# Kernel tuning notes

Measured on AMD Instinct MI355X. Metric: run time of the kernel, lower is better.

The kernel has to match this reference:

```python
import jax, jax.numpy as jnp
import numpy as np

FEATURE_DIM = 256
TEMP = 0.1
BASE_TEMP = 0.07
MAX_SAMPLES = 1024
SIM_THR = 0.7


def setup_inputs() -> dict:
    key = jax.random.key(0)
    ks = jax.random.split(key, 8)
    B, C, H, W = 4, FEATURE_DIM, 160, 160
    s = 1.0 / np.sqrt(C)
    return {
        'feats': jax.random.normal(ks[0], (B, C, H, W), jnp.float32),
        'labels': jax.random.randint(ks[1], (B, H, W), 0, 2).astype(jnp.int64),
        'superpixel_indice': jax.random.randint(ks[2], (B, H, W), 0, 200).astype(jnp.int64),
        'w1': jax.random.normal(ks[3], (C, C), jnp.float32) * s,
        'b1': jnp.zeros((C,), jnp.float32),
        'w2': jax.random.normal(ks[4], (C, C), jnp.float32) * s,
        'b2': jnp.zeros((C,), jnp.float32),
        'wa1': jax.random.normal(ks[5], (64, C), jnp.float32) * s,
        'ba1': jnp.zeros((64,), jnp.float32),
        'wa2': jax.random.normal(ks[6], (1, 64), jnp.float32) * (1.0 / 8.0),
        'ba2': jnp.zeros((1,), jnp.float32),
    }


def _per_sample(f, w, lab, sp):
    # f: (N, C) normalized proj feats, w: (N,) pixel weights, lab/sp: (N,) int
    valid = lab == 1
    # deterministic sample: stable-sort valid pixels to the front, take MAX_SAMPLES
    order = jnp.argsort(jnp.where(valid, 0, 1).astype(jnp.int32))
    idx = order[:MAX_SAMPLES]
    sel = valid[idx]                       # (S,) real-sample mask (pads if <S valid)
    tf = f[idx]                            # (S, C)
    tw = w[idx]                            # (S,)
    ts = sp[idx]                           # (S,)
    sim = tf @ tf.T                        # (S, S)
    S = MAX_SAMPLES
    eye = jnp.eye(S, dtype=bool)
    pos = (ts[:, None] == ts[None, :]) & (sim > SIM_THR)
    pos = pos & sel[:, None] & sel[None, :] & ~eye
    exp_sim = jnp.exp(sim / TEMP) * sel[None, :].astype(sim.dtype)
    denom = exp_sim.sum(axis=1)            # (S,)
    log_prob = sim / TEMP - jnp.log(jnp.where(denom > 0, denom, 1.0))[:, None]
    pw = tw[:, None] * tw[None, :]
    pwm = jnp.where(pos, pw, 0.0)
    psum = pwm.sum()
    loss = -(TEMP / BASE_TEMP) * (pwm * jnp.where(pos, log_prob, 0.0)).sum() / jnp.where(psum > 0, psum, 1.0)
    has = psum > 0
    return jnp.where(has, loss, 0.0), has


def reference(feats, labels, superpixel_indice, w1, b1, w2, b2, wa1, ba1, wa2, ba2):
    B, C, H, W = feats.shape
    x = jnp.transpose(feats, (0, 2, 3, 1)).reshape(B, H * W, C)  # (B, N, C)
    proj = jax.nn.relu(x @ w1.T + b1) @ w2.T + b2                # 1x1 convs == per-pixel matmul
    attn = jax.nn.sigmoid(jax.nn.relu(x @ wa1.T + ba1) @ wa2.T + ba2)[..., 0]  # (B, N)
    nrm = jnp.linalg.norm(proj, axis=-1, keepdims=True)
    fn = proj / jnp.maximum(nrm, 1e-12)
    lab = labels.reshape(B, -1)
    sp = superpixel_indice.reshape(B, -1)
    losses, flags = jax.vmap(_per_sample)(fn, attn, lab, sp)
    n = flags.sum().astype(jnp.float32)
    return jnp.where(n > 0, losses.sum() / jnp.maximum(n, 1.0), 0.0)
```

## Files before the change

### kernel.cpp

```cpp
#include <hip/hip_runtime.h>
#include <hip/hip_bf16.h>
#include <math.h>

#define NPIX   25600
#define CDIM   256
#define SSEL   1024
#define BATCH  4
#define NCHUNK 25
#define INV_T  10.0f
#define RATIO  1.4285714285714286f
#define THR    0.7f

typedef __attribute__((ext_vector_type(8))) short bf16x8;
typedef __attribute__((ext_vector_type(4))) float f32x4;
typedef unsigned short u16;

__device__ __forceinline__ u16 to_bf16(float v) {
  __hip_bfloat16 h = __float2bfloat16(v);
  return *reinterpret_cast<u16*>(&h);
}

__global__ __launch_bounds__(1024) void prep_kernel(
    const float* __restrict__ w1, const float* __restrict__ w2,
    const float* __restrict__ wa1,
    const int* __restrict__ labels, const int* __restrict__ sp,
    u16* __restrict__ w1b, u16* __restrict__ w2b, u16* __restrict__ wab,
    float* __restrict__ denom, float* __restrict__ Prow,
    float* __restrict__ Ssum,
    int* __restrict__ idx, int* __restrict__ selv, int* __restrict__ tsp) {
  __shared__ int wcnt[NCHUNK][16];
  __shared__ int cs[NCHUNK];
  int t = threadIdx.x;
  int blk = blockIdx.x;

  if (blk < BATCH * NCHUNK) {
    int b = blk / NCHUNK, ch = blk % NCHUNK;
    int lane = t & 63, wid = t >> 6;
    int my_isv = 0;
    unsigned long long my_mv = 0;
    for (int c = 0; c < NCHUNK; ++c) {
      int isv = (labels[b * NPIX + c * 1024 + t] == 1) ? 1 : 0;
      unsigned long long mv = __ballot(isv);
      if (c == ch) { my_isv = isv; my_mv = mv; }
      if (lane == 0) wcnt[c][wid] = __popcll(mv);
    }
    __syncthreads();
    if (t < NCHUNK) {
      int s = 0;
      for (int w = 0; w < 16; ++w) s += wcnt[t][w];
      cs[t] = s;
    }
    __syncthreads();
    int Vtot = 0, vbase = 0;
    for (int c = 0; c < NCHUNK; ++c) {
      int v = cs[c];
      Vtot += v;
      if (c < ch) vbase += v;
    }
    int ibase = ch * 1024 - vbase;
    int pv = __popcll(my_mv & ((1ull << lane) - 1ull));
    for (int w = 0; w < wid; ++w) pv += wcnt[ch][w];
    int i = ch * 1024 + t;
    int gslot = my_isv ? (vbase + pv) : (Vtot + ibase + (t - pv));
    if (gslot < SSEL) {
      idx [b * SSEL + gslot] = i;
      selv[b * SSEL + gslot] = my_isv;
      tsp [b * SSEL + gslot] = sp[b * NPIX + i];
    }
  } else {
    int e = (blk - BATCH * NCHUNK) * 1024 + t;
    w1b[e] = to_bf16(w1[e]);
    w2b[e] = to_bf16(w2[e]);
    if (e < 16384) wab[e] = to_bf16(wa1[e]);
    if (e < BATCH * SSEL) { denom[e] = 0.f; Prow[e] = 0.f; }
    if (e < BATCH) Ssum[e] = 0.f;
  }
}

__global__ __launch_bounds__(256) void mlp_fused(
    const float* __restrict__ feats, const int* __restrict__ idx,
    const u16* __restrict__ w1b, const u16* __restrict__ w2b,
    const u16* __restrict__ wab,
    const float* __restrict__ b1, const float* __restrict__ ba1,
    const float* __restrict__ wa2, const float* __restrict__ ba2,
    const float* __restrict__ b2,
    u16* __restrict__ fnb, float* __restrict__ tw) {
  int i0 = blockIdx.x * 16;
  int b  = i0 >> 10;
  int t  = threadIdx.x;
  int lane = t & 63, w = t >> 6, m = lane & 15, q = lane >> 4;

  __shared__ __align__(16) u16 xs[16 * 264];
  __shared__ __align__(16) u16 hs[16 * 264];
  __shared__ int ridx[16];
  __shared__ float ssl[4][16];

  if (t < 16) ridx[t] = idx[i0 + t];
  __syncthreads();

  const float* fb = feats + ((long)b * CDIM + t) * NPIX;
#pragma unroll
  for (int r = 0; r < 16; ++r)
    xs[r * 264 + t] = to_bf16(fb[ridx[r]]);
  __syncthreads();

  bf16x8 af[8];
#pragma unroll
  for (int ks = 0; ks < 8; ++ks)
    af[ks] = *(const bf16x8*)&xs[m * 264 + ks * 32 + q * 8];

  for (int g = w; g < 5; g += 4) {
    bool attn = (g == 4);
    const u16* bsrc = attn ? wab : (w1b + g * 64 * 256);
    f32x4 acc[4];
#pragma unroll
    for (int nt = 0; nt < 4; ++nt) acc[nt] = {0.f, 0.f, 0.f, 0.f};
#pragma unroll
    for (int ks = 0; ks < 8; ++ks) {
      int koff = ks * 32 + q * 8;
#pragma unroll
      for (int nt = 0; nt < 4; ++nt) {
        bf16x8 bh = *(const bf16x8*)&bsrc[(nt * 16 + m) * 256 + koff];
        acc[nt] = __builtin_amdgcn_mfma_f32_16x16x32_bf16(af[ks], bh, acc[nt], 0, 0, 0);
      }
    }
    if (!attn) {
#pragma unroll
      for (int nt = 0; nt < 4; ++nt) {
        int col = g * 64 + nt * 16 + m;
        float bb = b1[col];
#pragma unroll
        for (int reg = 0; reg < 4; ++reg)
          hs[(q * 4 + reg) * 264 + col] = to_bf16(fmaxf(acc[nt][reg] + bb, 0.f));
      }
    } else {
      float part[4] = {0.f, 0.f, 0.f, 0.f};
#pragma unroll
      for (int nt = 0; nt < 4; ++nt) {
        int ca = nt * 16 + m;
        float bb = ba1[ca], wv = wa2[ca];
#pragma unroll
        for (int reg = 0; reg < 4; ++reg)
          part[reg] += fmaxf(acc[nt][reg] + bb, 0.f) * wv;
      }
      for (int off = 8; off > 0; off >>= 1) {
#pragma unroll
        for (int reg = 0; reg < 4; ++reg)
          part[reg] += __shfl_xor(part[reg], off, 64);
      }
      if (m == 0) {
        float bb2 = ba2[0];
#pragma unroll
        for (int reg = 0; reg < 4; ++reg)
          tw[i0 + q * 4 + reg] = 1.f / (1.f + expf(-(part[reg] + bb2)));
      }
    }
  }
  __syncthreads();

  bf16x8 hf[8];
#pragma unroll
  for (int ks = 0; ks < 8; ++ks)
    hf[ks] = *(const bf16x8*)&hs[m * 264 + ks * 32 + q * 8];

  f32x4 acc2[4];
#pragma unroll
  for (int nt = 0; nt < 4; ++nt) acc2[nt] = {0.f, 0.f, 0.f, 0.f};
#pragma unroll
  for (int ks = 0; ks < 8; ++ks) {
    int koff = ks * 32 + q * 8;
#pragma unroll
    for (int nt = 0; nt < 4; ++nt) {
      bf16x8 bh = *(const bf16x8*)&w2b[(w * 64 + nt * 16 + m) * 256 + koff];
      acc2[nt] = __builtin_amdgcn_mfma_f32_16x16x32_bf16(hf[ks], bh, acc2[nt], 0, 0, 0);
    }
  }

  float ss[4] = {0.f, 0.f, 0.f, 0.f};
#pragma unroll
  for (int nt = 0; nt < 4; ++nt) {
    float bb = b2[w * 64 + nt * 16 + m];
#pragma unroll
    for (int reg = 0; reg < 4; ++reg) {
      float p = acc2[nt][reg] + bb;
      acc2[nt][reg] = p;
      ss[reg] += p * p;
    }
  }
  for (int off = 8; off > 0; off >>= 1) {
#pragma unroll
    for (int reg = 0; reg < 4; ++reg) ss[reg] += __shfl_xor(ss[reg], off, 64);
  }
  if (m == 0) {
#pragma unroll
    for (int reg = 0; reg < 4; ++reg) ssl[w][q * 4 + reg] = ss[reg];
  }
  __syncthreads();

  float inv[4];
#pragma unroll
  for (int reg = 0; reg < 4; ++reg) {
    int row = q * 4 + reg;
    float tot = ssl[0][row] + ssl[1][row] + ssl[2][row] + ssl[3][row];
    inv[reg] = 1.f / fmaxf(sqrtf(tot), 1e-12f);
  }

#pragma unroll
  for (int nt = 0; nt < 4; ++nt) {
    int col = w * 64 + nt * 16 + m;
#pragma unroll
    for (int reg = 0; reg < 4; ++reg)
      fnb[(i0 + q * 4 + reg) * 256 + col] = to_bf16(acc2[nt][reg] * inv[reg]);
  }
}

__global__ __launch_bounds__(256) void sim_kernel(
    const u16* __restrict__ fnb, const float* __restrict__ tw,
    const int* __restrict__ selv, const int* __restrict__ tsp,
    float* __restrict__ denom, float* __restrict__ Prow, float* __restrict__ Ssum) {
  int b = blockIdx.y;
  int t = threadIdx.x;
  int lane = t & 63, w = t >> 6;
  int m = lane & 15, q = lane >> 4;

  int rem = blockIdx.x, ti = 0;
  while (rem >= (16 - ti)) { rem -= (16 - ti); ++ti; }
  int tj = ti + rem;
  bool diag = (ti == tj);
  int i0 = ti * 64, j0 = tj * 64;
  int base = b << 10;

  __shared__ __align__(16) u16 Ah[64 * 72];
  __shared__ __align__(16) u16 Bhh[64 * 72];
  __shared__ float drl[64], Prl[64];
  __shared__ float dclw[4][64], Pclw[4][64];
  __shared__ float swv[4];

  const u16* Bh = diag ? Ah : Bhh;

  f32x4 acc[4];
#pragma unroll
  for (int nt = 0; nt < 4; ++nt) acc[nt] = {0.f, 0.f, 0.f, 0.f};

  for (int kk = 0; kk < 4; ++kk) {
    __syncthreads();
#pragma unroll
    for (int p = 0; p < 2; ++p) {
      int e = p * 256 + t;
      int row = e >> 3, kg = e & 7;
      int lo = row * 72 + kg * 8;
      *(uint4*)&Ah[lo] = *(const uint4*)&fnb[(base + i0 + row) * 256 + kk * 64 + kg * 8];
      if (!diag)
        *(uint4*)&Bhh[lo] = *(const uint4*)&fnb[(base + j0 + row) * 256 + kk * 64 + kg * 8];
    }
    __syncthreads();
#pragma unroll
    for (int ks = 0; ks < 2; ++ks) {
      int koff = ks * 32 + q * 8;
      bf16x8 ah = *(const bf16x8*)&Ah[(w * 16 + m) * 72 + koff];
#pragma unroll
      for (int nt = 0; nt < 4; ++nt) {
        bf16x8 bh = *(const bf16x8*)&Bh[(nt * 16 + m) * 72 + koff];
        acc[nt] = __builtin_amdgcn_mfma_f32_16x16x32_bf16(ah, bh, acc[nt], 0, 0, 0);
      }
    }
  }

  int   gi[4], gj[4], si[4], sj[4], ci[4], cj[4];
  float twi[4], twj[4];
#pragma unroll
  for (int reg = 0; reg < 4; ++reg) {
    int i = i0 + w * 16 + q * 4 + reg;
    gi[reg] = i; twi[reg] = tw[base + i];
    si[reg] = selv[base + i]; ci[reg] = tsp[base + i];
  }
#pragma unroll
  for (int nt = 0; nt < 4; ++nt) {
    int j = j0 + nt * 16 + m;
    gj[nt] = j; twj[nt] = tw[base + j];
    sj[nt] = selv[base + j]; cj[nt] = tsp[base + j];
  }

  float dR[4] = {0, 0, 0, 0}, PR[4] = {0, 0, 0, 0};
  float dC[4] = {0, 0, 0, 0}, PC[4] = {0, 0, 0, 0};
  float Sp = 0.f;
#pragma unroll
  for (int nt = 0; nt < 4; ++nt) {
#pragma unroll
    for (int reg = 0; reg < 4; ++reg) {
      float s = acc[nt][reg];
      float e10 = __expf(s * INV_T);
      if (sj[nt]) dR[reg] += e10;
      if (si[reg]) dC[nt] += e10;
      if (si[reg] && sj[nt] && (ci[reg] == cj[nt]) && (s > THR) && (gi[reg] != gj[nt])) {
        float pw = twi[reg] * twj[nt];
        PR[reg] += pw;
        PC[nt] += pw;
        Sp += pw * s;
      }
    }
  }

  for (int off = 8; off > 0; off >>= 1) {
#pragma unroll
    for (int reg = 0; reg < 4; ++reg) {
      dR[reg] += __shfl_xor(dR[reg], off, 64);
      PR[reg] += __shfl_xor(PR[reg], off, 64);
    }
  }
  if (m == 0) {
#pragma unroll
    for (int reg = 0; reg < 4; ++reg) {
      drl[w * 16 + q * 4 + reg] = dR[reg];
      Prl[w * 16 + q * 4 + reg] = PR[reg];
    }
  }
  if (!diag) {
    for (int off = 32; off >= 16; off >>= 1) {
#pragma unroll
      for (int nt = 0; nt < 4; ++nt) {
        dC[nt] += __shfl_xor(dC[nt], off, 64);
        PC[nt] += __shfl_xor(PC[nt], off, 64);
      }
    }
    if (q == 0) {
#pragma unroll
      for (int nt = 0; nt < 4; ++nt) {
        dclw[w][nt * 16 + m] = dC[nt];
        Pclw[w][nt * 16 + m] = PC[nt];
      }
    }
  }
  for (int off = 32; off > 0; off >>= 1) Sp += __shfl_xor(Sp, off, 64);
  if (lane == 0) swv[w] = Sp;
  __syncthreads();

  if (t < 64) {
    atomicAdd(&denom[base + i0 + t], drl[t]);
    atomicAdd(&Prow [base + i0 + t], Prl[t]);
    if (!diag) {
      float dc = dclw[0][t] + dclw[1][t] + dclw[2][t] + dclw[3][t];
      float pc = Pclw[0][t] + Pclw[1][t] + Pclw[2][t] + Pclw[3][t];
      atomicAdd(&denom[base + j0 + t], dc);
      atomicAdd(&Prow [base + j0 + t], pc);
    }
  }
  if (t == 0) {
    float St = swv[0] + swv[1] + swv[2] + swv[3];
    atomicAdd(&Ssum[b], diag ? St : 2.f * St);
  }
}

__global__ __launch_bounds__(1024) void finalize_kernel(
    const float* __restrict__ denom, const float* __restrict__ Prow,
    const float* __restrict__ Ssum, float* __restrict__ out) {
  int t = threadIdx.x;
  int b = t >> 8, u = t & 255;
  float P = 0.f, L = 0.f;
#pragma unroll
  for (int q = 0; q < 4; ++q) {
    int s = u + q * 256;
    float p = Prow[b * SSEL + s];
    float D = denom[b * SSEL + s];
    P += p;
    L += p * logf(D > 0.f ? D : 1.f);
  }
  for (int off = 32; off > 0; off >>= 1) {
    P += __shfl_xor(P, off, 64);
    L += __shfl_xor(L, off, 64);
  }
  __shared__ float wP[16], wL[16];
  int lane = t & 63, w = t >> 6;
  if (lane == 0) { wP[w] = P; wL[w] = L; }
  __syncthreads();
  if (t == 0) {
    float total = 0.f, n = 0.f;
    for (int bb = 0; bb < BATCH; ++bb) {
      float psum = wP[4 * bb] + wP[4 * bb + 1] + wP[4 * bb + 2] + wP[4 * bb + 3];
      float lsum = wL[4 * bb] + wL[4 * bb + 1] + wL[4 * bb + 2] + wL[4 * bb + 3];
      if (psum > 0.f) {
        float wls = Ssum[bb] * INV_T - lsum;
        total += -RATIO * wls / psum;
        n += 1.f;
      }
    }
    out[0] = (n > 0.f) ? (total / n) : 0.f;
  }
}

extern "C" void kernel_launch(void* const* d_in, const int* in_sizes, int n_in,
                              void* d_out, int out_size, void* d_ws, size_t ws_size,
                              hipStream_t stream) {
  const float* feats = (const float*)d_in[0];
  const int*   labels = (const int*)d_in[1];
  const int*   sp     = (const int*)d_in[2];
  const float* w1  = (const float*)d_in[3];
  const float* b1  = (const float*)d_in[4];
  const float* w2  = (const float*)d_in[5];
  const float* b2  = (const float*)d_in[6];
  const float* wa1 = (const float*)d_in[7];
  const float* ba1 = (const float*)d_in[8];
  const float* wa2 = (const float*)d_in[9];
  const float* ba2 = (const float*)d_in[10];
  float* out = (float*)d_out;

  char* W = (char*)d_ws;
  u16* w1b = (u16*)W;               W += 65536 * 2;
  u16* w2b = (u16*)W;               W += 65536 * 2;
  u16* wab = (u16*)W;               W += 16384 * 2;
  u16* fnb = (u16*)W;               W += 1048576 * 2;
  float* tw   = (float*)W;          W += 4096 * 4;
  float* denom= (float*)W;          W += 4096 * 4;
  float* Prow = (float*)W;          W += 4096 * 4;
  float* Ssum = (float*)W;          W += 4 * 4;
  int*   idx  = (int*)W;            W += 4096 * 4;
  int*   selv = (int*)W;            W += 4096 * 4;
  int*   tsp  = (int*)W;            W += 4096 * 4;

  prep_kernel<<<BATCH * NCHUNK + 64, 1024, 0, stream>>>(
      w1, w2, wa1, labels, sp, w1b, w2b, wab, denom, Prow, Ssum,
      idx, selv, tsp);
  mlp_fused<<<256, 256, 0, stream>>>(feats, idx, w1b, w2b, wab,
                                     b1, ba1, wa2, ba2, b2, fnb, tw);
  sim_kernel<<<dim3(136, BATCH), 256, 0, stream>>>(fnb, tw, selv, tsp,
                                                   denom, Prow, Ssum);
  finalize_kernel<<<1, 1024, 0, stream>>>(denom, Prow, Ssum, out);
}
```

Baseline: 189.9 us.

## Compact valid pixels with one block per batch and remap feature gather threads

The selection prefix-scan in prep_kernel now runs one block per batch that loops over all chunks, instead of 25 blocks per batch that each re-read every label chunk. This removes redundant label reads, but each batch's scan is now serial across chunks. The feature gather in mlp_fused now assigns each thread one sample pixel and 16 channels rather than one channel and 16 pixels. This changes the address pattern of the strided gather from feats.

```diff
diff --git a/kernel.cpp b/kernel.cpp
--- a/kernel.cpp
+++ b/kernel.cpp
@@ -28,20 +28,17 @@
     float* __restrict__ denom, float* __restrict__ Prow,
     float* __restrict__ Ssum,
     int* __restrict__ idx, int* __restrict__ selv, int* __restrict__ tsp) {
-  __shared__ int wcnt[NCHUNK][16];
-  __shared__ int cs[NCHUNK];
   int t = threadIdx.x;
   int blk = blockIdx.x;
 
-  if (blk < BATCH * NCHUNK) {
-    int b = blk / NCHUNK, ch = blk % NCHUNK;
+  if (blk < BATCH) {
+    __shared__ int wcnt[NCHUNK][16];
+    __shared__ int cs[NCHUNK];
+    int b = blk;
     int lane = t & 63, wid = t >> 6;
-    int my_isv = 0;
-    unsigned long long my_mv = 0;
     for (int c = 0; c < NCHUNK; ++c) {
       int isv = (labels[b * NPIX + c * 1024 + t] == 1) ? 1 : 0;
       unsigned long long mv = __ballot(isv);
-      if (c == ch) { my_isv = isv; my_mv = mv; }
       if (lane == 0) wcnt[c][wid] = __popcll(mv);
     }
     __syncthreads();
@@ -51,24 +48,26 @@
       cs[t] = s;
     }
     __syncthreads();
-    int Vtot = 0, vbase = 0;
+    int Vtot = 0;
+    for (int c = 0; c < NCHUNK; ++c) Vtot += cs[c];
+    int vbase = 0;
     for (int c = 0; c < NCHUNK; ++c) {
-      int v = cs[c];
-      Vtot += v;
-      if (c < ch) vbase += v;
-    }
-    int ibase = ch * 1024 - vbase;
-    int pv = __popcll(my_mv & ((1ull << lane) - 1ull));
-    for (int w = 0; w < wid; ++w) pv += wcnt[ch][w];
-    int i = ch * 1024 + t;
-    int gslot = my_isv ? (vbase + pv) : (Vtot + ibase + (t - pv));
-    if (gslot < SSEL) {
-      idx [b * SSEL + gslot] = i;
-      selv[b * SSEL + gslot] = my_isv;
-      tsp [b * SSEL + gslot] = sp[b * NPIX + i];
+      int i = c * 1024 + t;
+      int isv = (labels[b * NPIX + i] == 1) ? 1 : 0;
+      unsigned long long mv = __ballot(isv);
+      int pv = __popcll(mv & ((1ull << lane) - 1ull));
+      for (int w = 0; w < wid; ++w) pv += wcnt[c][w];
+      int ibase = c * 1024 - vbase;
+      int gslot = isv ? (vbase + pv) : (Vtot + ibase + (t - pv));
+      if (gslot < SSEL) {
+        idx [b * SSEL + gslot] = i;
+        selv[b * SSEL + gslot] = isv;
+        tsp [b * SSEL + gslot] = sp[b * NPIX + i];
+      }
+      vbase += cs[c];
     }
   } else {
-    int e = (blk - BATCH * NCHUNK) * 1024 + t;
+    int e = (blk - BATCH) * 1024 + t;
     w1b[e] = to_bf16(w1[e]);
     w2b[e] = to_bf16(w2[e]);
     if (e < 16384) wab[e] = to_bf16(wa1[e]);
@@ -98,10 +97,16 @@
   if (t < 16) ridx[t] = idx[i0 + t];
   __syncthreads();
 
-  const float* fb = feats + ((long)b * CDIM + t) * NPIX;
-#pragma unroll
-  for (int r = 0; r < 16; ++r)
-    xs[r * 264 + t] = to_bf16(fb[ridx[r]]);
+  {
+    int s = t & 15, cg = t >> 4;
+    int pix = ridx[s];
+    const float* fb = feats + (long)b * CDIM * NPIX + pix;
+#pragma unroll
+    for (int cc = 0; cc < 16; ++cc) {
+      int c = cg * 16 + cc;
+      xs[s * 264 + c] = to_bf16(fb[(long)c * NPIX]);
+    }
+  }
   __syncthreads();
 
   bf16x8 af[8];
@@ -417,7 +422,7 @@
   int*   selv = (int*)W;            W += 4096 * 4;
   int*   tsp  = (int*)W;            W += 4096 * 4;
 
-  prep_kernel<<<BATCH * NCHUNK + 64, 1024, 0, stream>>>(
+  prep_kernel<<<BATCH + 64, 1024, 0, stream>>>(
       w1, w2, wa1, labels, sp, w1b, w2b, wab, denom, Prow, Ssum,
       idx, selv, tsp);
   mlp_fused<<<256, 256, 0, stream>>>(feats, idx, w1b, w2b, wab,
```

New measurement: 200.2 us. 1.05x slower.
